# Kernel tuning notes

Hardware: AMD Instinct MI355X
Metric: run time of the kernel (lower is better)

The kernel has to match this reference:

```python
import jax, jax.numpy as jnp
from jax import lax
import numpy as np


def _box_sum(x, k):
    # zero-padded sliding-window sum over last two dims of [B, H, W];
    # 'SAME' padding with additive identity 0 exactly matches nn.Unfold's
    # zero padding of k//2 on each side for odd k.
    return lax.reduce_window(x, 0.0, lax.add, (1, k, k), (1, 1, 1), 'SAME')


def _local_std(x, k):
    # torch.std over the k*k patch dim is the unbiased (n-1) sample std;
    # fused one-pass form: var = (sum(x^2) - sum(x)^2/n) / (n-1)
    n = float(k * k)
    s1 = _box_sum(x, k)
    s2 = _box_sum(x * x, k)
    var = (s2 - s1 * s1 / n) / (n - 1.0)
    return jnp.sqrt(jnp.maximum(var, 0.0))


def setup_inputs() -> dict:
    key = jax.random.key(0)
    k1, k2 = jax.random.split(key)
    B, C, H, W = 8, 6, 1024, 1024
    predictions = jax.random.normal(k1, (B, C, H, W), dtype=jnp.float32)
    targets = jax.random.randint(k2, (B, H, W), 0, C, dtype=jnp.int64)
    return {"predictions": predictions, "targets": targets, "kernel_size": 5}


def reference(predictions, targets, kernel_size):
    k = int(kernel_size)
    pred_classes = jnp.argmax(predictions, axis=1).astype(jnp.float32)  # [B,H,W]
    tgt = targets.astype(jnp.float32)                                    # [B,H,W]
    pred_consistency = _local_std(pred_classes, k)
    target_consistency = _local_std(tgt, k)
    return jnp.mean((pred_consistency - target_consistency) ** 2)
```

## Files before the change

### kernel.cpp

```cpp
#include <hip/hip_runtime.h>

#define IMG_H 1024
#define IMG_W 1024
#define HW    (IMG_H * IMG_W)
#define NCLS  6
#define NBATCH 8
#define TW 64
#define TH 32

__global__ __launch_bounds__(256) void argmax_kernel(
    const float* __restrict__ pred, unsigned char* __restrict__ cls) {
  const int idx = blockIdx.x * blockDim.x + threadIdx.x;
  const int b  = idx >> 18;
  const int p4 = idx & 0x3FFFF;
  const float4* base = (const float4*)pred + (size_t)b * NCLS * (HW / 4) + p4;
  float4 best = base[0];
  int ix = 0, iy = 0, iz = 0, iw = 0;
#pragma unroll
  for (int c = 1; c < NCLS; ++c) {
    float4 v = base[(size_t)c * (HW / 4)];
    if (v.x > best.x) { best.x = v.x; ix = c; }
    if (v.y > best.y) { best.y = v.y; iy = c; }
    if (v.z > best.z) { best.z = v.z; iz = c; }
    if (v.w > best.w) { best.w = v.w; iw = c; }
  }
  ((uchar4*)cls)[idx] = make_uchar4((unsigned char)ix, (unsigned char)iy,
                                    (unsigned char)iz, (unsigned char)iw);
}

__global__ __launch_bounds__(256) void loss_kernel(
    const unsigned char* __restrict__ cls, const int* __restrict__ tgt,
    float* __restrict__ out) {
  __shared__ uint2 halo[(TH + 4) * (TW + 4)];
  __shared__ uint2 colsum[TH * (TW + 4)];
  __shared__ float wsum[4];

  const int b   = blockIdx.z;
  const int ty0 = blockIdx.y * TH;
  const int tx0 = blockIdx.x * TW;
  const size_t ibase = (size_t)b * HW;

  for (int i = threadIdx.x; i < (TH + 4) * (TW + 4); i += 256) {
    const int hy = i / (TW + 4);
    const int hx = i - hy * (TW + 4);
    const int gy = ty0 + hy - 2;
    const int gx = tx0 + hx - 2;
    uint2 v = make_uint2(0u, 0u);
    if ((unsigned)gy < IMG_H && (unsigned)gx < IMG_W) {
      const size_t gi = ibase + (size_t)gy * IMG_W + gx;
      const unsigned p = cls[gi];
      const unsigned t = (unsigned)tgt[gi];
      v.x = p | ((p * p) << 16);
      v.y = t | ((t * t) << 16);
    }
    halo[i] = v;
  }
  __syncthreads();

  for (int i = threadIdx.x; i < TH * (TW + 4); i += 256) {
    uint2 s = halo[i];
#pragma unroll
    for (int dy = 1; dy < 5; ++dy) {
      const uint2 a = halo[i + dy * (TW + 4)];
      s.x += a.x;
      s.y += a.y;
    }
    colsum[i] = s;
  }
  __syncthreads();

  float acc = 0.f;
  for (int i = threadIdx.x; i < TH * TW; i += 256) {
    const int y = i >> 6;
    const int x = i & 63;
    const int ci = y * (TW + 4) + x;
    uint2 s = colsum[ci];
#pragma unroll
    for (int dx = 1; dx < 5; ++dx) {
      const uint2 a = colsum[ci + dx];
      s.x += a.x;
      s.y += a.y;
    }
    const int s1p = (int)(s.x & 0xFFFFu), s2p = (int)(s.x >> 16);
    const int s1t = (int)(s.y & 0xFFFFu), s2t = (int)(s.y >> 16);
    const float varp = (float)(25 * s2p - s1p * s1p) * (1.0f / 600.0f);
    const float vart = (float)(25 * s2t - s1t * s1t) * (1.0f / 600.0f);
    const float d = sqrtf(varp) - sqrtf(vart);
    acc += d * d;
  }

#pragma unroll
  for (int off = 32; off > 0; off >>= 1) acc += __shfl_down(acc, off, 64);
  const int lane = threadIdx.x & 63;
  const int wid  = threadIdx.x >> 6;
  if (lane == 0) wsum[wid] = acc;
  __syncthreads();
  if (threadIdx.x == 0) {
    const float t = wsum[0] + wsum[1] + wsum[2] + wsum[3];
    atomicAdd(out, t * (1.0f / 8388608.0f));
  }
}

extern "C" void kernel_launch(void* const* d_in, const int* in_sizes, int n_in,
                              void* d_out, int out_size, void* d_ws, size_t ws_size,
                              hipStream_t stream) {
  const float* pred = (const float*)d_in[0];
  const int* tgt    = (const int*)d_in[1];
  float* out = (float*)d_out;
  unsigned char* cls = (unsigned char*)d_ws;

  hipMemsetAsync(d_out, 0, sizeof(float), stream);

  argmax_kernel<<<dim3(NBATCH * HW / 4 / 256), dim3(256), 0, stream>>>(pred, cls);

  dim3 grid(IMG_W / TW, IMG_H / TH, NBATCH);
  loss_kernel<<<grid, dim3(256), 0, stream>>>(cls, tgt, out);
}
```

Measured before the change: 351.4 us.

## Fuse argmax into loss kernel, computing class indices during halo load

Drops the separate argmax kernel and its byte-sized class buffer in workspace. The loss kernel now computes the argmax over the six channels directly while loading each halo element. This removes one launch and the write and re-read of the class map. In exchange, halo pixels (about 20% extra for a 68x36 tile over 64x32) re-read all six prediction channels, and the loads are scalar rather than float4, which may hurt coalescing efficiency.

```diff
diff --git a/kernel.cpp b/kernel.cpp
--- a/kernel.cpp
+++ b/kernel.cpp
@@ -7,61 +7,51 @@
 #define NBATCH 8
 #define TW 64
 #define TH 32
+#define HXW (TW + 4)
+#define HXH (TH + 4)
 
-__global__ __launch_bounds__(256) void argmax_kernel(
-    const float* __restrict__ pred, unsigned char* __restrict__ cls) {
-  const int idx = blockIdx.x * blockDim.x + threadIdx.x;
-  const int b  = idx >> 18;
-  const int p4 = idx & 0x3FFFF;
-  const float4* base = (const float4*)pred + (size_t)b * NCLS * (HW / 4) + p4;
-  float4 best = base[0];
-  int ix = 0, iy = 0, iz = 0, iw = 0;
-#pragma unroll
-  for (int c = 1; c < NCLS; ++c) {
-    float4 v = base[(size_t)c * (HW / 4)];
-    if (v.x > best.x) { best.x = v.x; ix = c; }
-    if (v.y > best.y) { best.y = v.y; iy = c; }
-    if (v.z > best.z) { best.z = v.z; iz = c; }
-    if (v.w > best.w) { best.w = v.w; iw = c; }
-  }
-  ((uchar4*)cls)[idx] = make_uchar4((unsigned char)ix, (unsigned char)iy,
-                                    (unsigned char)iz, (unsigned char)iw);
-}
-
-__global__ __launch_bounds__(256) void loss_kernel(
-    const unsigned char* __restrict__ cls, const int* __restrict__ tgt,
+__global__ __launch_bounds__(256) void fused_loss_kernel(
+    const float* __restrict__ pred, const int* __restrict__ tgt,
     float* __restrict__ out) {
-  __shared__ uint2 halo[(TH + 4) * (TW + 4)];
-  __shared__ uint2 colsum[TH * (TW + 4)];
+  __shared__ uint2 halo[HXH * HXW];
+  __shared__ uint2 colsum[TH * HXW];
   __shared__ float wsum[4];
 
   const int b   = blockIdx.z;
   const int ty0 = blockIdx.y * TH;
   const int tx0 = blockIdx.x * TW;
   const size_t ibase = (size_t)b * HW;
+  const float* pbase = pred + (size_t)b * NCLS * HW;
 
-  for (int i = threadIdx.x; i < (TH + 4) * (TW + 4); i += 256) {
-    const int hy = i / (TW + 4);
-    const int hx = i - hy * (TW + 4);
+  for (int i = threadIdx.x; i < HXH * HXW; i += 256) {
+    const int hy = i / HXW;
+    const int hx = i - hy * HXW;
     const int gy = ty0 + hy - 2;
     const int gx = tx0 + hx - 2;
     uint2 v = make_uint2(0u, 0u);
     if ((unsigned)gy < IMG_H && (unsigned)gx < IMG_W) {
-      const size_t gi = ibase + (size_t)gy * IMG_W + gx;
-      const unsigned p = cls[gi];
-      const unsigned t = (unsigned)tgt[gi];
-      v.x = p | ((p * p) << 16);
-      v.y = t | ((t * t) << 16);
+      const size_t pi = (size_t)gy * IMG_W + gx;
+      const float* p = pbase + pi;
+      float best = p[0];
+      unsigned c0 = 0;
+#pragma unroll
+      for (int c = 1; c < NCLS; ++c) {
+        const float vv = p[(size_t)c * HW];
+        if (vv > best) { best = vv; c0 = (unsigned)c; }
+      }
+      const unsigned t = (unsigned)tgt[ibase + pi];
+      v.x = c0 | ((c0 * c0) << 16);
+      v.y = t  | ((t * t) << 16);
     }
     halo[i] = v;
   }
   __syncthreads();
 
-  for (int i = threadIdx.x; i < TH * (TW + 4); i += 256) {
+  for (int i = threadIdx.x; i < TH * HXW; i += 256) {
     uint2 s = halo[i];
 #pragma unroll
     for (int dy = 1; dy < 5; ++dy) {
-      const uint2 a = halo[i + dy * (TW + 4)];
+      const uint2 a = halo[i + dy * HXW];
       s.x += a.x;
       s.y += a.y;
     }
@@ -73,7 +63,7 @@
   for (int i = threadIdx.x; i < TH * TW; i += 256) {
     const int y = i >> 6;
     const int x = i & 63;
-    const int ci = y * (TW + 4) + x;
+    const int ci = y * HXW + x;
     uint2 s = colsum[ci];
 #pragma unroll
     for (int dx = 1; dx < 5; ++dx) {
@@ -107,12 +97,10 @@
   const float* pred = (const float*)d_in[0];
   const int* tgt    = (const int*)d_in[1];
   float* out = (float*)d_out;
-  unsigned char* cls = (unsigned char*)d_ws;
+  (void)d_ws; (void)ws_size;
 
   hipMemsetAsync(d_out, 0, sizeof(float), stream);
 
-  argmax_kernel<<<dim3(NBATCH * HW / 4 / 256), dim3(256), 0, stream>>>(pred, cls);
-
   dim3 grid(IMG_W / TW, IMG_H / TH, NBATCH);
-  loss_kernel<<<grid, dim3(256), 0, stream>>>(cls, tgt, out);
+  fused_loss_kernel<<<grid, dim3(256), 0, stream>>>(pred, tgt, out);
 }
```

Measured after the change: 328.7 us. 1.07x faster.
